# Kernel tuning notes

Hardware: AMD Instinct MI355X
Metric: run time of the kernel (lower is better)

Reference implementation:

```python
import jax, jax.numpy as jnp
import numpy as np

N, E, C = 50000, 300000, 128


def _line_graph(src, dst, n):
    # PyG LineGraph(force_directed=True): line-graph node per edge; edge j -> edge i iff dst(j) == src(i)
    order = np.argsort(src, kind='stable')          # edges grouped by src node
    deg_out = np.bincount(src, minlength=n)
    ptr = np.concatenate([np.zeros(1, np.int64), np.cumsum(deg_out)])
    counts = deg_out[dst]                           # #successor edges of each edge j
    total = int(counts.sum())
    line_src = np.repeat(np.arange(src.shape[0], dtype=np.int64), counts)
    grp_start = np.repeat(ptr[dst], counts)
    cum = np.cumsum(counts)
    within = np.arange(total, dtype=np.int64) - np.repeat(cum - counts, counts)
    line_dst = order[grp_start + within]
    return np.stack([line_src, line_dst]).astype(np.int32)


def setup_inputs() -> dict:
    rng = np.random.default_rng(0)
    ei = rng.integers(0, N, size=(2, E), dtype=np.int64)
    line_ei = _line_graph(ei[0], ei[1], N)
    key = jax.random.key(0)
    k = jax.random.split(key, 6)
    s_e = float(1.0 / np.sqrt(3 * C))  # torch Linear init bound
    s_g = float(1.0 / np.sqrt(C))
    return {
        "x": jax.random.normal(k[0], (N, C), jnp.float32),
        "edge_attr": jax.random.normal(k[1], (E, C), jnp.float32),
        "W_edge": jax.random.uniform(k[2], (3 * C, C), jnp.float32, -s_e, s_e),
        "b_edge": jax.random.uniform(k[3], (C,), jnp.float32, -s_e, s_e),
        "W_gcn": jax.random.uniform(k[4], (C, C), jnp.float32, -s_g, s_g),
        "b_gcn": jnp.zeros((C,), jnp.float32),
        "edge_index": jnp.asarray(ei, dtype=jnp.int32),
        "batch": jnp.zeros((N,), jnp.int32),
        "line_edge_index": jnp.asarray(line_ei),
    }


def reference(x, edge_attr, W_edge, b_edge, W_gcn, b_gcn,
              edge_index, batch, line_edge_index):
    src, dst = edge_index[0], edge_index[1]
    # gather endpoints, concat with edge_attr, linear 3C -> C
    merged = jnp.concatenate([x[src], x[dst], edge_attr], axis=1)    # [E, 3C]
    line_x = merged @ W_edge + b_edge                                # [E, C] line-graph node feats

    # GCNConv with self loops on the line graph (line-graph nodes = original edges)
    e = line_x.shape[0]
    loops = jnp.arange(e, dtype=line_edge_index.dtype)
    row = jnp.concatenate([line_edge_index[0], loops])
    col = jnp.concatenate([line_edge_index[1], loops])
    xw = line_x @ W_gcn                                              # [E, C]
    deg = jax.ops.segment_sum(jnp.ones(row.shape, xw.dtype), col, num_segments=e)
    dinv = jnp.where(deg > 0, jax.lax.rsqrt(deg), 0.0)
    norm = dinv[row] * dinv[col]                                     # [M+E]
    out = jax.ops.segment_sum(xw[row] * norm[:, None], col, num_segments=e) + b_gcn
    return jax.nn.leaky_relu(out)  # negative_slope = 0.01 (torch default)
```

## Files before the change

### kernel.cpp

```cpp
#include <hip/hip_runtime.h>
#include <hip/hip_bf16.h>


typedef __bf16 bf16x8 __attribute__((ext_vector_type(8)));
typedef float  f32x4  __attribute__((ext_vector_type(4)));

#define C_DIM 128

__device__ __forceinline__ float bfu_lo(unsigned u) { return __uint_as_float(u << 16); }
__device__ __forceinline__ float bfu_hi(unsigned u) { return __uint_as_float(u & 0xffff0000u); }
__device__ __forceinline__ unsigned bf16_bits(float f) {
    __bf16 h = (__bf16)f;
    return (unsigned)__builtin_bit_cast(unsigned short, h);
}

__global__ void k_wcomb(const float* __restrict__ W_edge, const float* __restrict__ W_gcn,
                        const float* __restrict__ b_edge,
                        __bf16* __restrict__ Wf, float* __restrict__ b_comb) {
    int idx = blockIdx.x * 256 + threadIdx.x;
    if (idx < 384 * 128) {
        int k = idx >> 7, c = idx & 127;
        float s = 0.f;
        for (int m = 0; m < 128; ++m) s += W_edge[k * 128 + m] * W_gcn[m * 128 + c];
        int ks = k >> 5, kc8 = (k >> 3) & 3, j = k & 7;
        int col16 = c >> 4, c15 = c & 15;
        Wf[(size_t)(((ks * 8 + col16) * 64) + kc8 * 16 + c15) * 8 + j] = (__bf16)s;
    }
    if (blockIdx.x == 0 && threadIdx.x < 128) {
        int c = threadIdx.x;
        float s = 0.f;
        for (int m = 0; m < 128; ++m) s += b_edge[m] * W_gcn[m * 128 + c];
        b_comb[c] = s;
    }
}

__global__ void k_indeg(const int* __restrict__ dst, int E, int* __restrict__ indeg) {
    int e = blockIdx.x * 256 + threadIdx.x;
    if (e < E) atomicAdd(&indeg[dst[e]], 1);
}

__global__ void k_scan_bsum(const int* __restrict__ indeg, int n, int* __restrict__ bsum) {
    __shared__ int ws[16];
    int i = blockIdx.x * 1024 + threadIdx.x;
    int v = (i < n) ? indeg[i] : 0;
    int lane = threadIdx.x & 63, wid = threadIdx.x >> 6;
    for (int off = 32; off; off >>= 1) v += __shfl_down(v, off);
    if (lane == 0) ws[wid] = v;
    __syncthreads();
    if (threadIdx.x < 16) {
        int s = ws[threadIdx.x];
        for (int off = 8; off; off >>= 1) s += __shfl_down(s, off);
        if (threadIdx.x == 0) bsum[blockIdx.x] = s;
    }
}

__global__ void k_scan_top(int* __restrict__ bsum, int nb, int n, int* __restrict__ ptr) {
    int lane = threadIdx.x;
    int v = (lane < nb) ? bsum[lane] : 0;
    int incl = v;
    for (int off = 1; off < 64; off <<= 1) {
        int t = __shfl_up(incl, off);
        if (lane >= off) incl += t;
    }
    if (lane < nb) bsum[lane] = incl - v;
    if (lane == 63) ptr[n] = incl;
}

__global__ void k_scan_fin(const int* __restrict__ indeg, int n, const int* __restrict__ bsum,
                           int* __restrict__ ptr, int* __restrict__ cursor) {
    __shared__ int wsum[16];
    int i = blockIdx.x * 1024 + threadIdx.x;
    int v = (i < n) ? indeg[i] : 0;
    int lane = threadIdx.x & 63, wid = threadIdx.x >> 6;
    int incl = v;
    for (int off = 1; off < 64; off <<= 1) {
        int t = __shfl_up(incl, off);
        if (lane >= off) incl += t;
    }
    if (lane == 63) wsum[wid] = incl;
    __syncthreads();
    if (wid == 0 && lane < 16) {
        int s = wsum[lane];
        for (int off = 1; off < 16; off <<= 1) {
            int t = __shfl_up(s, off);
            if (lane >= off) s += t;
        }
        wsum[lane] = s;
    }
    __syncthreads();
    int woff = wid ? wsum[wid - 1] : 0;
    if (i < n) {
        int ex = bsum[blockIdx.x] + woff + incl - v;
        ptr[i] = ex;
        cursor[i] = ex;
    }
}

__global__ void k_place(const int* __restrict__ dst, int E,
                        int* __restrict__ cursor, int* __restrict__ adj) {
    int e = blockIdx.x * 256 + threadIdx.x;
    if (e < E) {
        int pos = atomicAdd(&cursor[dst[e]], 1);
        adj[pos] = e;
    }
}

__global__ __launch_bounds__(256) void k_p12(
    const float* __restrict__ x, const __bf16* __restrict__ Wf,
    const float* __restrict__ b_comb,
    __bf16* __restrict__ P1, __bf16* __restrict__ P2, int M) {

    __shared__ __align__(16) __bf16 As[64 * 136];

    const int tid = threadIdx.x;
    const int mbase = blockIdx.x * 64;
    const int r = tid >> 2, q = tid & 3;
    const int m_r = mbase + r;
    const int m_rc = (m_r < M) ? m_r : 0;
    const float* rp = x + (size_t)m_rc * C_DIM;

#pragma unroll
    for (int s4 = 0; s4 < 4; ++s4) {
        const float* p = rp + s4 * 32 + q * 8;
        float4 f0 = *(const float4*)p;
        float4 f1 = *(const float4*)(p + 4);
        bf16x8 h;
        h[0] = (__bf16)f0.x; h[1] = (__bf16)f0.y; h[2] = (__bf16)f0.z; h[3] = (__bf16)f0.w;
        h[4] = (__bf16)f1.x; h[5] = (__bf16)f1.y; h[6] = (__bf16)f1.z; h[7] = (__bf16)f1.w;
        int u = s4 * 4 + q;
        *(bf16x8*)&As[r * 128 + ((u ^ (r & 7)) << 3)] = h;
    }
    __syncthreads();

    const int lane = tid & 63, wid = tid >> 6;
    const int wr = wid >> 1, wc = wid & 1;
    const int kc8 = lane >> 4;
    const int arow0 = wr * 32 + (lane & 15);
    const int arow1 = arow0 + 16;
    const __bf16* wfb = Wf + ((size_t)(wc * 4) * 64 + lane) * 8;

    f32x4 acc1[2][4] = {};
    f32x4 acc2[2][4] = {};

#pragma unroll
    for (int ks = 0; ks < 4; ++ks) {
        int u = ks * 4 + kc8;
        bf16x8 a0 = *(const bf16x8*)&As[arow0 * 128 + ((u ^ (arow0 & 7)) << 3)];
        bf16x8 a1 = *(const bf16x8*)&As[arow1 * 128 + ((u ^ (arow1 & 7)) << 3)];
#pragma unroll
        for (int n = 0; n < 4; ++n) {
            bf16x8 b1 = *(const bf16x8*)&wfb[(size_t)(ks * 8 + n) * 64 * 8];
            bf16x8 b2 = *(const bf16x8*)&wfb[(size_t)((ks + 4) * 8 + n) * 64 * 8];
            acc1[0][n] = __builtin_amdgcn_mfma_f32_16x16x32_bf16(a0, b1, acc1[0][n], 0, 0, 0);
            acc1[1][n] = __builtin_amdgcn_mfma_f32_16x16x32_bf16(a1, b1, acc1[1][n], 0, 0, 0);
            acc2[0][n] = __builtin_amdgcn_mfma_f32_16x16x32_bf16(a0, b2, acc2[0][n], 0, 0, 0);
            acc2[1][n] = __builtin_amdgcn_mfma_f32_16x16x32_bf16(a1, b2, acc2[1][n], 0, 0, 0);
        }
    }

#pragma unroll
    for (int pass = 0; pass < 2; ++pass) {
        __syncthreads();
#pragma unroll
        for (int m = 0; m < 2; ++m)
#pragma unroll
            for (int j = 0; j < 4; ++j) {
                int row = wr * 32 + m * 16 + (lane >> 4) * 4 + j;
#pragma unroll
                for (int n = 0; n < 4; ++n) {
                    int c = wc * 64 + n * 16 + (lane & 15);
                    float v = pass == 0 ? acc1[m][n][j] + b_comb[c] : acc2[m][n][j];
                    As[row * 136 + c] = (__bf16)v;
                }
            }
        __syncthreads();
        if (m_r < M) {
            __bf16* outp = (pass == 0 ? P1 : P2) + (size_t)m_r * C_DIM + q * 32;
#pragma unroll
            for (int i = 0; i < 4; ++i)
                *(bf16x8*)(outp + i * 8) = *(const bf16x8*)&As[r * 136 + q * 32 + i * 8];
        }
    }
}

__global__ __launch_bounds__(256) void k_gemm3(
    const float* __restrict__ ea, const __bf16* __restrict__ Wf,
    const __bf16* __restrict__ P1, const __bf16* __restrict__ P2,
    const int* __restrict__ src, const int* __restrict__ dst,
    const int* __restrict__ indeg, __bf16* __restrict__ xws, int E) {

    __shared__ __align__(16) __bf16 As[64 * 136];

    const int tid = threadIdx.x;
    const int ebase = blockIdx.x * 64;
    const int r = tid >> 2, q = tid & 3;
    const int e_r = ebase + r;
    const int e_rc = (e_r < E) ? e_r : 0;
    const float* rp = ea + (size_t)e_rc * C_DIM;

    const int s_e = src[e_rc], d_e = dst[e_rc];
    const float di = rsqrtf(1.0f + (float)indeg[s_e]);
    uint4 g1[4], g2[4];
    {
        const uint4* p1 = (const uint4*)(P1 + (size_t)s_e * C_DIM + q * 32);
        const uint4* p2 = (const uint4*)(P2 + (size_t)d_e * C_DIM + q * 32);
#pragma unroll
        for (int i = 0; i < 4; ++i) { g1[i] = p1[i]; g2[i] = p2[i]; }
    }

#pragma unroll
    for (int s4 = 0; s4 < 4; ++s4) {
        const float* p = rp + s4 * 32 + q * 8;
        float4 f0 = *(const float4*)p;
        float4 f1 = *(const float4*)(p + 4);
        bf16x8 h;
        h[0] = (__bf16)f0.x; h[1] = (__bf16)f0.y; h[2] = (__bf16)f0.z; h[3] = (__bf16)f0.w;
        h[4] = (__bf16)f1.x; h[5] = (__bf16)f1.y; h[6] = (__bf16)f1.z; h[7] = (__bf16)f1.w;
        int u = s4 * 4 + q;
        *(bf16x8*)&As[r * 128 + ((u ^ (r & 7)) << 3)] = h;
    }
    __syncthreads();

    const int lane = tid & 63, wid = tid >> 6;
    const int wr = wid >> 1, wc = wid & 1;
    const int kc8 = lane >> 4;
    const int arow0 = wr * 32 + (lane & 15);
    const int arow1 = arow0 + 16;
    const __bf16* wfb = Wf + ((size_t)(8 * 8 + wc * 4) * 64 + lane) * 8;

    f32x4 acc[2][4] = {};

#pragma unroll
    for (int ks = 0; ks < 4; ++ks) {
        int u = ks * 4 + kc8;
        bf16x8 a0 = *(const bf16x8*)&As[arow0 * 128 + ((u ^ (arow0 & 7)) << 3)];
        bf16x8 a1 = *(const bf16x8*)&As[arow1 * 128 + ((u ^ (arow1 & 7)) << 3)];
#pragma unroll
        for (int n = 0; n < 4; ++n) {
            bf16x8 b = *(const bf16x8*)&wfb[(size_t)(ks * 8 + n) * 64 * 8];
            acc[0][n] = __builtin_amdgcn_mfma_f32_16x16x32_bf16(a0, b, acc[0][n], 0, 0, 0);
            acc[1][n] = __builtin_amdgcn_mfma_f32_16x16x32_bf16(a1, b, acc[1][n], 0, 0, 0);
        }
    }

    __syncthreads();
#pragma unroll
    for (int m = 0; m < 2; ++m)
#pragma unroll
        for (int j = 0; j < 4; ++j) {
            int row = wr * 32 + m * 16 + (lane >> 4) * 4 + j;
#pragma unroll
            for (int n = 0; n < 4; ++n) {
                int c = wc * 64 + n * 16 + (lane & 15);
                As[row * 136 + c] = (__bf16)acc[m][n][j];
            }
        }
    __syncthreads();
    if (e_r < E) {
        __bf16* outp = xws + (size_t)e_r * C_DIM + q * 32;
#pragma unroll
        for (int i = 0; i < 4; ++i) {
            bf16x8 a8 = *(const bf16x8*)&As[r * 136 + q * 32 + i * 8];
            bf16x8 h1 = __builtin_bit_cast(bf16x8, g1[i]);
            bf16x8 h2 = __builtin_bit_cast(bf16x8, g2[i]);
            bf16x8 o;
#pragma unroll
            for (int j = 0; j < 8; ++j)
                o[j] = (__bf16)(((float)a8[j] + (float)h1[j] + (float)h2[j]) * di);
            *(bf16x8*)(outp + i * 8) = o;
        }
    }
}

__global__ void k_agg(const __bf16* __restrict__ xws, const int* __restrict__ ptr,
                      const int* __restrict__ adj, __bf16* __restrict__ agg, int Nn) {
    int v = blockIdx.x * 4 + (threadIdx.x >> 6);
    if (v >= Nn) return;
    int c = threadIdx.x & 63;
    int b0 = ptr[v], b1 = ptr[v + 1];
    float s0 = 0.f, s1 = 0.f;
    for (int t = b0; t < b1; ++t) {
        int j = adj[t];
        unsigned u = *(const unsigned*)(xws + (size_t)j * C_DIM + c * 2);
        s0 += bfu_lo(u);
        s1 += bfu_hi(u);
    }
    unsigned o = bf16_bits(s0) | (bf16_bits(s1) << 16);
    *(unsigned*)(agg + (size_t)v * C_DIM + c * 2) = o;
}

__global__ void k_out(const __bf16* __restrict__ xws, const __bf16* __restrict__ agg,
                      const int* __restrict__ src, const int* __restrict__ indeg,
                      const float* __restrict__ b_gcn, float* __restrict__ out, int E) {
    int g = blockIdx.x * 256 + threadIdx.x;
    if (g >= E * (C_DIM / 4)) return;
    int e = g >> 5, c4 = (g & 31) * 4;
    int s = src[e];
    float di = rsqrtf(1.0f + (float)indeg[s]);
    uint2 u = *(const uint2*)(xws + (size_t)e * C_DIM + c4);
    uint2 au = *(const uint2*)(agg + (size_t)s * C_DIM + c4);
    float4 b = *(const float4*)&b_gcn[c4];
    float4 r;
    r.x = di * (bfu_lo(au.x) + bfu_lo(u.x)) + b.x;
    r.y = di * (bfu_hi(au.x) + bfu_hi(u.x)) + b.y;
    r.z = di * (bfu_lo(au.y) + bfu_lo(u.y)) + b.z;
    r.w = di * (bfu_hi(au.y) + bfu_hi(u.y)) + b.w;
    r.x = r.x > 0.f ? r.x : 0.01f * r.x;
    r.y = r.y > 0.f ? r.y : 0.01f * r.y;
    r.z = r.z > 0.f ? r.z : 0.01f * r.z;
    r.w = r.w > 0.f ? r.w : 0.01f * r.w;
    *(float4*)&out[(size_t)e * C_DIM + c4] = r;
}

extern "C" void kernel_launch(void* const* d_in, const int* in_sizes, int n_in,
                              void* d_out, int out_size, void* d_ws, size_t ws_size,
                              hipStream_t stream) {
    const float* x      = (const float*)d_in[0];
    const float* ea     = (const float*)d_in[1];
    const float* W_edge = (const float*)d_in[2];
    const float* b_edge = (const float*)d_in[3];
    const float* W_gcn  = (const float*)d_in[4];
    const float* b_gcn  = (const float*)d_in[5];
    const int*   ei     = (const int*)d_in[6];

    const int C  = in_sizes[3];
    const int Nn = in_sizes[0] / C;
    const int E  = in_sizes[1] / C;
    const int* srcp = ei;
    const int* dstp = ei + E;

    char* ws = (char*)d_ws;
    size_t off = 0;
    auto alloc = [&](size_t bytes) { size_t o = off; off = (off + bytes + 255) & ~(size_t)255; return o; };
    __bf16* Wf     = (__bf16*)(ws + alloc((size_t)384 * 128 * sizeof(__bf16)));
    float*  b_comb = (float*)(ws + alloc(128 * sizeof(float)));
    int*    indeg  = (int*)(ws + alloc((size_t)Nn * sizeof(int)));
    int*    ptr    = (int*)(ws + alloc((size_t)(Nn + 1) * sizeof(int)));
    int*    cursor = (int*)(ws + alloc((size_t)Nn * sizeof(int)));
    int*    bsum   = (int*)(ws + alloc(64 * sizeof(int)));
    int*    adj    = (int*)(ws + alloc((size_t)E * sizeof(int)));
    __bf16* P1     = (__bf16*)(ws + alloc((size_t)Nn * C * sizeof(__bf16)));
    __bf16* P2     = (__bf16*)(ws + alloc((size_t)Nn * C * sizeof(__bf16)));
    __bf16* xws    = (__bf16*)(ws + alloc((size_t)E * C * sizeof(__bf16)));
    __bf16* agg    = (__bf16*)(ws + alloc((size_t)Nn * C * sizeof(__bf16)));

    const int nb = (Nn + 1023) / 1024;

    (void)hipMemsetAsync(indeg, 0, (size_t)Nn * sizeof(int), stream);
    k_wcomb<<<192, 256, 0, stream>>>(W_edge, W_gcn, b_edge, Wf, b_comb);
    k_indeg<<<(E + 255) / 256, 256, 0, stream>>>(dstp, E, indeg);
    k_scan_bsum<<<nb, 1024, 0, stream>>>(indeg, Nn, bsum);
    k_scan_top<<<1, 64, 0, stream>>>(bsum, nb, Nn, ptr);
    k_scan_fin<<<nb, 1024, 0, stream>>>(indeg, Nn, bsum, ptr, cursor);
    k_place<<<(E + 255) / 256, 256, 0, stream>>>(dstp, E, cursor, adj);
    k_p12<<<(Nn + 63) / 64, 256, 0, stream>>>(x, Wf, b_comb, P1, P2, Nn);
    k_gemm3<<<(E + 63) / 64, 256, 0, stream>>>(ea, Wf, P1, P2, srcp, dstp, indeg, xws, E);
    k_agg<<<(Nn + 3) / 4, 256, 0, stream>>>(xws, ptr, adj, agg, Nn);
    k_out<<<(E * (C / 4) + 255) / 256, 256, 0, stream>>>(xws, agg, srcp, indeg, b_gcn, (float*)d_out, E);
}
```

Baseline: 235.7 us.

## Make edge GEMM wave-independent with direct global A loads and per-wave LDS

Each wavefront in the fused edge-attribute GEMM kernel now owns 16 edges and all 128 output columns. It loads its edge_attr rows straight from global memory into MFMA A-operand registers instead of staging a 64-row tile through shared memory. The output transpose uses a small per-wave LDS buffer, which removes every block-wide __syncthreads. The aim is to cut barrier stalls and LDS traffic. In exchange, each wave reads twice as many weight fragments, the A-operand global loads are less coalesced, and the per-row bounds check is gone, which assumes E is a multiple of 16.

```diff
diff --git a/kernel.cpp b/kernel.cpp
--- a/kernel.cpp
+++ b/kernel.cpp
@@ -189,86 +189,61 @@
     const int* __restrict__ src, const int* __restrict__ dst,
     const int* __restrict__ indeg, __bf16* __restrict__ xws, int E) {
 
-    __shared__ __align__(16) __bf16 As[64 * 136];
+    __shared__ __align__(16) __bf16 Ls[4][16 * 132];
 
     const int tid = threadIdx.x;
-    const int ebase = blockIdx.x * 64;
-    const int r = tid >> 2, q = tid & 3;
-    const int e_r = ebase + r;
-    const int e_rc = (e_r < E) ? e_r : 0;
-    const float* rp = ea + (size_t)e_rc * C_DIM;
-
-    const int s_e = src[e_rc], d_e = dst[e_rc];
+    const int wid = tid >> 6, lane = tid & 63;
+    const int ebase = (blockIdx.x * 4 + wid) * 16;
+    if (ebase >= E) return;
+
+    const int rr = lane & 15;
+    const int kc = lane >> 4;
+    const int e = ebase + rr;
+
+    const int s_e = src[e], d_e = dst[e];
     const float di = rsqrtf(1.0f + (float)indeg[s_e]);
-    uint4 g1[4], g2[4];
-    {
-        const uint4* p1 = (const uint4*)(P1 + (size_t)s_e * C_DIM + q * 32);
-        const uint4* p2 = (const uint4*)(P2 + (size_t)d_e * C_DIM + q * 32);
-#pragma unroll
-        for (int i = 0; i < 4; ++i) { g1[i] = p1[i]; g2[i] = p2[i]; }
-    }
-
-#pragma unroll
-    for (int s4 = 0; s4 < 4; ++s4) {
-        const float* p = rp + s4 * 32 + q * 8;
-        float4 f0 = *(const float4*)p;
-        float4 f1 = *(const float4*)(p + 4);
-        bf16x8 h;
-        h[0] = (__bf16)f0.x; h[1] = (__bf16)f0.y; h[2] = (__bf16)f0.z; h[3] = (__bf16)f0.w;
-        h[4] = (__bf16)f1.x; h[5] = (__bf16)f1.y; h[6] = (__bf16)f1.z; h[7] = (__bf16)f1.w;
-        int u = s4 * 4 + q;
-        *(bf16x8*)&As[r * 128 + ((u ^ (r & 7)) << 3)] = h;
-    }
-    __syncthreads();
-
-    const int lane = tid & 63, wid = tid >> 6;
-    const int wr = wid >> 1, wc = wid & 1;
-    const int kc8 = lane >> 4;
-    const int arow0 = wr * 32 + (lane & 15);
-    const int arow1 = arow0 + 16;
-    const __bf16* wfb = Wf + ((size_t)(8 * 8 + wc * 4) * 64 + lane) * 8;
-
-    f32x4 acc[2][4] = {};
+
+    const float* ap = ea + (size_t)e * C_DIM + kc * 8;
+
+    f32x4 acc[8] = {};
+    const __bf16* wfl = Wf + (size_t)(8 * 8) * 64 * 8 + (size_t)lane * 8;
 
 #pragma unroll
     for (int ks = 0; ks < 4; ++ks) {
-        int u = ks * 4 + kc8;
-        bf16x8 a0 = *(const bf16x8*)&As[arow0 * 128 + ((u ^ (arow0 & 7)) << 3)];
-        bf16x8 a1 = *(const bf16x8*)&As[arow1 * 128 + ((u ^ (arow1 & 7)) << 3)];
-#pragma unroll
-        for (int n = 0; n < 4; ++n) {
-            bf16x8 b = *(const bf16x8*)&wfb[(size_t)(ks * 8 + n) * 64 * 8];
-            acc[0][n] = __builtin_amdgcn_mfma_f32_16x16x32_bf16(a0, b, acc[0][n], 0, 0, 0);
-            acc[1][n] = __builtin_amdgcn_mfma_f32_16x16x32_bf16(a1, b, acc[1][n], 0, 0, 0);
+        float4 f0 = *(const float4*)(ap + ks * 32);
+        float4 f1 = *(const float4*)(ap + ks * 32 + 4);
+        bf16x8 a;
+        a[0] = (__bf16)f0.x; a[1] = (__bf16)f0.y; a[2] = (__bf16)f0.z; a[3] = (__bf16)f0.w;
+        a[4] = (__bf16)f1.x; a[5] = (__bf16)f1.y; a[6] = (__bf16)f1.z; a[7] = (__bf16)f1.w;
+#pragma unroll
+        for (int n = 0; n < 8; ++n) {
+            bf16x8 b = *(const bf16x8*)(wfl + (size_t)(ks * 8 + n) * 512);
+            acc[n] = __builtin_amdgcn_mfma_f32_16x16x32_bf16(a, b, acc[n], 0, 0, 0);
         }
     }
 
-    __syncthreads();
-#pragma unroll
-    for (int m = 0; m < 2; ++m)
-#pragma unroll
-        for (int j = 0; j < 4; ++j) {
-            int row = wr * 32 + m * 16 + (lane >> 4) * 4 + j;
-#pragma unroll
-            for (int n = 0; n < 4; ++n) {
-                int c = wc * 64 + n * 16 + (lane & 15);
-                As[row * 136 + c] = (__bf16)acc[m][n][j];
-            }
-        }
-    __syncthreads();
-    if (e_r < E) {
-        __bf16* outp = xws + (size_t)e_r * C_DIM + q * 32;
-#pragma unroll
-        for (int i = 0; i < 4; ++i) {
-            bf16x8 a8 = *(const bf16x8*)&As[r * 136 + q * 32 + i * 8];
-            bf16x8 h1 = __builtin_bit_cast(bf16x8, g1[i]);
-            bf16x8 h2 = __builtin_bit_cast(bf16x8, g2[i]);
-            bf16x8 o;
-#pragma unroll
-            for (int j = 0; j < 8; ++j)
-                o[j] = (__bf16)(((float)a8[j] + (float)h1[j] + (float)h2[j]) * di);
-            *(bf16x8*)(outp + i * 8) = o;
-        }
+    const bf16x8* p1 = (const bf16x8*)(P1 + (size_t)s_e * C_DIM + kc * 32);
+    const bf16x8* p2 = (const bf16x8*)(P2 + (size_t)d_e * C_DIM + kc * 32);
+    bf16x8 h1[4], h2[4];
+#pragma unroll
+    for (int i = 0; i < 4; ++i) { h1[i] = p1[i]; h2[i] = p2[i]; }
+
+    __bf16* lw = Ls[wid];
+#pragma unroll
+    for (int n = 0; n < 8; ++n)
+#pragma unroll
+        for (int j = 0; j < 4; ++j)
+            lw[(kc * 4 + j) * 132 + n * 16 + rr] = (__bf16)acc[n][j];
+
+    __bf16* op = xws + (size_t)e * C_DIM + kc * 32;
+#pragma unroll
+    for (int i = 0; i < 4; ++i) {
+        bf16x8 a8 = *(const bf16x8*)&lw[rr * 132 + kc * 32 + i * 8];
+        bf16x8 o;
+#pragma unroll
+        for (int j = 0; j < 8; ++j)
+            o[j] = (__bf16)(((float)a8[j] + (float)h1[i][j] + (float)h2[i][j]) * di);
+        *(bf16x8*)(op + i * 8) = o;
     }
 }
 
```

New measurement: 255.3 us. 1.08x slower.
